# Performance work log

Measured on AMD Instinct MI355X. Metric: run time of the kernel, lower is better.

Reference implementation:

```python
import jax, jax.numpy as jnp
import numpy as np

N = 100000
E = 1600000
D = 128
H = 64
C = 10
G = 1024  # number of graphs in the batch


def setup_inputs() -> dict:
    key = jax.random.key(0)
    ks = jax.random.split(key, 12)
    x = jax.random.normal(ks[0], (N, D), dtype=jnp.float32)
    edge_index = jax.random.randint(ks[1], (2, E), 0, N, dtype=jnp.int64)
    batch = jnp.sort(jax.random.randint(ks[2], (N,), 0, G, dtype=jnp.int64))
    def glorot(k, fan_in, fan_out):
        s = jnp.sqrt(6.0 / (fan_in + fan_out))
        return jax.random.uniform(k, (fan_in, fan_out), jnp.float32, -s, s)
    W1 = glorot(ks[3], D, H); b1 = jnp.zeros((H,), jnp.float32)
    W2 = glorot(ks[4], H, H); b2 = jnp.zeros((H,), jnp.float32)
    W3 = glorot(ks[5], H, H); b3 = jnp.zeros((H,), jnp.float32)
    Wl = glorot(ks[6], H, C); bl = jnp.zeros((C,), jnp.float32)
    return {"x": x, "edge_index": edge_index, "batch": batch,
            "W1": W1, "b1": b1, "W2": W2, "b2": b2,
            "W3": W3, "b3": b3, "Wl": Wl, "bl": bl}


def gcn_conv(x, row, col, dinv, W, b):
    # PyG GCNConv: x' = D^-1/2 (A + I) D^-1/2 (x W) + b
    xw = x @ W                                   # (N, H)
    norm = dinv[row] * dinv[col]                 # (E+N,)
    msg = xw[row] * norm[:, None]                # gather + scale
    out = jax.ops.segment_sum(msg, col, num_segments=N)
    return out + b


def reference(x, edge_index, batch, W1, b1, W2, b2, W3, b3, Wl, bl):
    # add self loops once; normalization coefficients shared by all layers
    loop = jnp.arange(N, dtype=edge_index.dtype)
    row = jnp.concatenate([edge_index[0], loop])
    col = jnp.concatenate([edge_index[1], loop])
    deg = jax.ops.segment_sum(jnp.ones_like(col, dtype=x.dtype), col, num_segments=N)
    dinv = jnp.where(deg > 0, jax.lax.rsqrt(deg), 0.0)

    h = gcn_conv(x, row, col, dinv, W1, b1)
    h = gcn_conv(h, row, col, dinv, W2, b2)
    h = gcn_conv(h, row, col, dinv, W3, b3)

    # global mean pool over graphs
    sums = jax.ops.segment_sum(h, batch, num_segments=G)          # (G, H)
    cnts = jax.ops.segment_sum(jnp.ones((N,), h.dtype), batch, num_segments=G)
    pooled = sums / jnp.maximum(cnts, 1.0)[:, None]

    # dropout(p=0.5) is identity in eval mode
    return pooled @ Wl + bl                                        # (G, C)
```

## Files before the change

kernel.cpp:

```cpp
#include <hip/hip_runtime.h>

#define NN 100000
#define EE 1600000
#define DI 128
#define HH 64
#define CO 10
#define PADF 16
#define GG 1024
#define BSH 7
#define BNODES 128
#define NB ((NN + BNODES - 1) / BNODES)
#define TILE 4096
#define NT ((EE + TILE - 1) / TILE)
#define SN (NB * NT)
#define SCB 1024
#define NSB ((SN + SCB - 1) / SCB)
#define LPN 4
#define BT 256

__global__ __launch_bounds__(256) void k_front(const int* __restrict__ col,
                                               const float* __restrict__ W1, const float* __restrict__ W2,
                                               const float* __restrict__ W3, const float* __restrict__ Wl,
                                               const float* __restrict__ b1, const float* __restrict__ b2,
                                               const float* __restrict__ b3,
                                               const int* __restrict__ batch,
                                               int* __restrict__ cnt, float* __restrict__ Wf,
                                               float* __restrict__ cvec, int* __restrict__ gstart) {
    __shared__ float smem[1280];
    int bid = blockIdx.x, t = threadIdx.x;
    if (bid < NT) {
        int* h = (int*)smem;
        for (int i = t; i < NB; i += 256) h[i] = 0;
        __syncthreads();
        int base = bid * TILE, end = min(base + TILE, EE);
        for (int e = base + t; e < end; e += 256)
            atomicAdd(&h[__builtin_nontemporal_load(&col[e]) >> BSH], 1);
        __syncthreads();
        for (int i = t; i < NB; i += 256) cnt[i * NT + bid] = h[i];
    } else if (bid == NT) {
        float* M3l = smem;
        float* M23l = smem + 640;
        for (int i = t; i < HH * CO; i += 256) {
            int r = i / CO, c = i % CO; float s = 0.f;
            for (int k = 0; k < HH; ++k) s += W3[r * HH + k] * Wl[k * CO + c];
            M3l[i] = s;
        }
        __syncthreads();
        for (int i = t; i < HH * CO; i += 256) {
            int r = i / CO, c = i % CO; float s = 0.f;
            for (int k = 0; k < HH; ++k) s += W2[r * HH + k] * M3l[k * CO + c];
            M23l[i] = s;
        }
        __syncthreads();
        for (int i = t; i < DI * CO; i += 256) {
            int r = i / CO, c = i % CO; float s = 0.f;
            for (int k = 0; k < HH; ++k) s += W1[r * HH + k] * M23l[k * CO + c];
            Wf[i] = s;
        }
        if (t < CO) {
            float s1 = 0.f, s2 = 0.f, s3 = 0.f;
            for (int k = 0; k < HH; ++k) {
                s1 += b1[k] * M23l[k * CO + t];
                s2 += b2[k] * M3l[k * CO + t];
                s3 += b3[k] * Wl[k * CO + t];
            }
            cvec[t] = s1; cvec[CO + t] = s2; cvec[2 * CO + t] = s3;
        }
    } else {
        int g = (bid - NT - 1) * 256 + t;
        if (g <= GG) {
            int lo = 0, hi = NN;
            while (lo < hi) { int mid = (lo + hi) >> 1; if (batch[mid] < g) lo = mid + 1; else hi = mid; }
            gstart[g] = lo;
        }
    }
}

__global__ __launch_bounds__(SCB) void k_scanA(int* __restrict__ a, int* __restrict__ bsum) {
    __shared__ int s[SCB];
    int t = threadIdx.x, idx = blockIdx.x * SCB + t;
    int v = (idx < SN) ? a[idx] : 0;
    s[t] = v;
    __syncthreads();
    for (int off = 1; off < SCB; off <<= 1) {
        int u = (t >= off) ? s[t - off] : 0;
        __syncthreads();
        s[t] += u;
        __syncthreads();
    }
    if (idx < SN) a[idx] = s[t] - v;
    if (t == SCB - 1) bsum[blockIdx.x] = s[t];
}
__global__ __launch_bounds__(SCB) void k_scanC(int* __restrict__ a, const int* __restrict__ bsum) {
    __shared__ int red[SCB];
    int t = threadIdx.x, bid = blockIdx.x;
    int partial = 0;
    for (int i = t; i < bid; i += SCB) partial += bsum[i];
    red[t] = partial;
    __syncthreads();
    for (int off = SCB / 2; off > 0; off >>= 1) {
        if (t < off) red[t] += red[t + off];
        __syncthreads();
    }
    int idx = bid * SCB + t;
    if (idx < SN) a[idx] += red[0];
}

__global__ __launch_bounds__(256) void k_sxw(const int* __restrict__ row, const int* __restrict__ col,
                                             const int* __restrict__ S, unsigned* __restrict__ ebuf,
                                             const float* __restrict__ x, const float* __restrict__ Wf,
                                             float* __restrict__ as_) {
    __shared__ float smf[DI * CO];
    int* smi = (int*)smf;
    int bid = blockIdx.x, t = threadIdx.x;
    if (bid < NT) {
        for (int i = t; i < NB; i += 256) smi[i] = S[i * NT + bid];
        __syncthreads();
        int base = bid * TILE, end = min(base + TILE, EE);
        for (int e = base + t; e < end; e += 256) {
            int c = __builtin_nontemporal_load(&col[e]);
            int r = __builtin_nontemporal_load(&row[e]);
            int pos = atomicAdd(&smi[c >> BSH], 1);
            ebuf[pos] = ((unsigned)r << BSH) | (unsigned)(c & (BNODES - 1));
        }
    } else {
        for (int i = t; i < DI * CO; i += 256) smf[i] = Wf[i];
        __syncthreads();
        int gid = (bid - NT) * 256 + t;
        if (gid >= NN) return;
        int pr = gid >> 1, c0 = (gid & 1) * 5;
        int n0 = 2 * pr, n1 = n0 + 1;
        float a0[5] = {0, 0, 0, 0, 0}, a1[5] = {0, 0, 0, 0, 0};
        const float4* x0 = (const float4*)(x + (size_t)n0 * DI);
        const float4* x1 = (const float4*)(x + (size_t)n1 * DI);
#pragma unroll 4
        for (int d4 = 0; d4 < DI / 4; ++d4) {
            float4 u = x0[d4], v = x1[d4];
            const float* w = &smf[d4 * 4 * CO + c0];
#pragma unroll
            for (int c = 0; c < 5; ++c) {
                float w0 = w[c], w1 = w[CO + c], w2 = w[2 * CO + c], w3 = w[3 * CO + c];
                a0[c] += u.x * w0 + u.y * w1 + u.z * w2 + u.w * w3;
                a1[c] += v.x * w0 + v.y * w1 + v.z * w2 + v.w * w3;
            }
        }
        float* r0 = as_ + (size_t)n0 * PADF + c0;
        float* r1 = as_ + (size_t)n1 * PADF + c0;
#pragma unroll
        for (int c = 0; c < 5; ++c) { r0[c] = a0[c]; r1[c] = a1[c]; }
    }
}

__global__ __launch_bounds__(256) void k_bsort(const unsigned* __restrict__ ebuf, const int* __restrict__ S,
                                               int* __restrict__ srcIdx, int* __restrict__ rowptr_end,
                                               float* __restrict__ dinv) {
    __shared__ int cnt[BNODES];
    __shared__ int s[BNODES];
    __shared__ int ofs[BNODES];
    int t = threadIdx.x;
    int b = blockIdx.x;
    if (t < BNODES) cnt[t] = 0;
    __syncthreads();
    int beg = S[b * NT];
    int end = (b + 1 < NB) ? S[(b + 1) * NT] : EE;
    for (int e = beg + t; e < end; e += 256)
        atomicAdd(&cnt[__builtin_nontemporal_load(&ebuf[e]) & (BNODES - 1)], 1);
    __syncthreads();
    int v = 0;
    if (t < BNODES) { v = cnt[t]; s[t] = v; }
    __syncthreads();
    for (int off = 1; off < BNODES; off <<= 1) {
        int u = 0;
        if (t < BNODES && t >= off) u = s[t - off];
        __syncthreads();
        if (t < BNODES) s[t] += u;
        __syncthreads();
    }
    if (t < BNODES) {
        int n = (b << BSH) + t;
        if (n < NN) {
            dinv[n] = rsqrtf((float)(v + 1));
            rowptr_end[n] = beg + s[t];
        }
        ofs[t] = beg + s[t] - v;
    }
    __syncthreads();
    for (int e = beg + t; e < end; e += 256) {
        unsigned p = __builtin_nontemporal_load(&ebuf[e]);
        int pos = atomicAdd(&ofs[p & (BNODES - 1)], 1);
        srcIdx[pos] = (int)(p >> BSH);
    }
}

template <int MODE>
__global__ __launch_bounds__(256) void k_gather(const int* __restrict__ rowptr_end,
                                                const int* __restrict__ srcIdx,
                                                const float* __restrict__ src,
                                                const float* __restrict__ dinv,
                                                const float* __restrict__ cvec, int coff,
                                                float* __restrict__ dst) {
    int gid = blockIdx.x * 256 + threadIdx.x;
    int n = gid >> 2;
    int l = threadIdx.x & (LPN - 1);
    if (n >= NN) return;
    int beg = (n == 0) ? 0 : rowptr_end[n - 1];
    int end = rowptr_end[n];
    float acc[CO];
#pragma unroll
    for (int c = 0; c < CO; ++c) acc[c] = 0.f;
    for (int e = beg + l; e < end; e += LPN) {
        int s = __builtin_nontemporal_load(&srcIdx[e]);
        const float* sp = src + (size_t)s * PADF;
        float4 a = ((const float4*)sp)[0];
        float4 b = ((const float4*)sp)[1];
        float2 c2 = ((const float2*)(sp + 8))[0];
        if (MODE == 0) {
            float w = dinv[s];
            acc[0] += w * a.x; acc[1] += w * a.y; acc[2] += w * a.z; acc[3] += w * a.w;
            acc[4] += w * b.x; acc[5] += w * b.y; acc[6] += w * b.z; acc[7] += w * b.w;
            acc[8] += w * c2.x; acc[9] += w * c2.y;
        } else {
            acc[0] += a.x; acc[1] += a.y; acc[2] += a.z; acc[3] += a.w;
            acc[4] += b.x; acc[5] += b.y; acc[6] += b.z; acc[7] += b.w;
            acc[8] += c2.x; acc[9] += c2.y;
        }
    }
#pragma unroll
    for (int m = 1; m < LPN; m <<= 1) {
#pragma unroll
        for (int c = 0; c < CO; ++c) acc[c] += __shfl_xor(acc[c], m, 64);
    }
    if (l == 0) {
        float di = dinv[n];
        const float* selfp = src + (size_t)n * PADF;
        float4 sa = ((const float4*)selfp)[0];
        float4 sb = ((const float4*)selfp)[1];
        float2 sc = ((const float2*)(selfp + 8))[0];
        float self[CO] = {sa.x, sa.y, sa.z, sa.w, sb.x, sb.y, sb.z, sb.w, sc.x, sc.y};
        float o[CO];
#pragma unroll
        for (int c = 0; c < CO; ++c) {
            float sv = (MODE == 0) ? di * self[c] : self[c];
            float y = di * (acc[c] + sv) + cvec[coff + c];
            o[c] = (MODE == 2) ? y : y * di;
        }
        float* dp = dst + (size_t)n * PADF;
        ((float4*)dp)[0] = make_float4(o[0], o[1], o[2], o[3]);
        ((float4*)dp)[1] = make_float4(o[4], o[5], o[6], o[7]);
        ((float2*)(dp + 8))[0] = make_float2(o[8], o[9]);
    }
}

__global__ __launch_bounds__(64) void k_pool(const float* __restrict__ h,
                                             const int* __restrict__ gstart,
                                             const float* __restrict__ bl,
                                             float* __restrict__ out) {
    int g = blockIdx.x;
    int beg = gstart[g], end = gstart[g + 1];
    int l = threadIdx.x;
    float acc[CO];
#pragma unroll
    for (int c = 0; c < CO; ++c) acc[c] = 0.f;
    for (int n = beg + l; n < end; n += 64) {
        const float* sp = h + (size_t)n * PADF;
        float4 a = ((const float4*)sp)[0];
        float4 b = ((const float4*)sp)[1];
        float2 c2 = ((const float2*)(sp + 8))[0];
        acc[0] += a.x; acc[1] += a.y; acc[2] += a.z; acc[3] += a.w;
        acc[4] += b.x; acc[5] += b.y; acc[6] += b.z; acc[7] += b.w;
        acc[8] += c2.x; acc[9] += c2.y;
    }
#pragma unroll
    for (int m = 1; m < 64; m <<= 1) {
#pragma unroll
        for (int c = 0; c < CO; ++c) acc[c] += __shfl_xor(acc[c], m, 64);
    }
    if (l == 0) {
        float cf = fmaxf((float)(end - beg), 1.f);
#pragma unroll
        for (int c = 0; c < CO; ++c) out[(size_t)g * CO + c] = acc[c] / cf + bl[c];
    }
}

extern "C" void kernel_launch(void* const* d_in, const int* in_sizes, int n_in,
                              void* d_out, int out_size, void* d_ws, size_t ws_size,
                              hipStream_t stream) {
    const float* x    = (const float*)d_in[0];
    const int*   ei   = (const int*)d_in[1];
    const int*   batch= (const int*)d_in[2];
    const float* W1   = (const float*)d_in[3];
    const float* b1   = (const float*)d_in[4];
    const float* W2   = (const float*)d_in[5];
    const float* b2   = (const float*)d_in[6];
    const float* W3   = (const float*)d_in[7];
    const float* b3   = (const float*)d_in[8];
    const float* Wl   = (const float*)d_in[9];
    const float* bl   = (const float*)d_in[10];
    float* out = (float*)d_out;

    const int* row = ei;
    const int* col = ei + EE;

    float* ws = (float*)d_ws;
    size_t off = 0;
    auto alloc = [&](size_t elems) { size_t cur = off; off += (elems + 63) & ~(size_t)63; return cur; };
    float*    Wf      = ws + alloc(DI * CO);
    float*    cvec    = ws + alloc(3 * CO);
    float*    dinv    = ws + alloc(NN);
    int*      S       = (int*)(ws + alloc(SN));
    int*      bsum    = (int*)(ws + alloc(NSB + 64));
    unsigned* ebuf    = (unsigned*)(ws + alloc(EE));
    int*      srcIdx  = (int*)(ws + alloc(EE));
    int*      rowptr  = (int*)(ws + alloc(NN));
    float*    as_     = ws + alloc((size_t)NN * PADF);
    float*    bbuf    = ws + alloc((size_t)NN * PADF);
    int*      gstart  = (int*)(ws + alloc(GG + 1));
    (void)ws_size; (void)in_sizes; (void)n_in; (void)out_size;

    int gNL = ((NN * LPN) + BT - 1) / BT;
    int gFront = NT + 1 + (GG + 1 + BT - 1) / BT;
    int gSxw = NT + (NN + BT - 1) / BT;

    hipLaunchKernelGGL(k_front,    dim3(gFront), dim3(BT), 0, stream,
                       col, W1, W2, W3, Wl, b1, b2, b3, batch, S, Wf, cvec, gstart);
    hipLaunchKernelGGL(k_scanA,    dim3(NSB), dim3(SCB), 0, stream, S, bsum);
    hipLaunchKernelGGL(k_scanC,    dim3(NSB), dim3(SCB), 0, stream, S, bsum);
    hipLaunchKernelGGL(k_sxw,      dim3(gSxw), dim3(BT), 0, stream, row, col, S, ebuf, x, Wf, as_);
    hipLaunchKernelGGL(k_bsort,    dim3(NB),  dim3(BT), 0, stream, ebuf, S, srcIdx, rowptr, dinv);

    hipLaunchKernelGGL((k_gather<0>), dim3(gNL), dim3(BT), 0, stream, rowptr, srcIdx, as_,  dinv, cvec, 0,      bbuf);
    hipLaunchKernelGGL((k_gather<1>), dim3(gNL), dim3(BT), 0, stream, rowptr, srcIdx, bbuf, dinv, cvec, CO,     as_);
    hipLaunchKernelGGL((k_gather<2>), dim3(gNL), dim3(BT), 0, stream, rowptr, srcIdx, as_,  dinv, cvec, 2 * CO, bbuf);

    hipLaunchKernelGGL(k_pool, dim3(GG), dim3(64), 0, stream, bbuf, gstart, bl, out);
}
```

Baseline: 288.8 us.

## Split gather by feature quarter per lane instead of by edge

The gather kernel now gives each of the four lanes per node one float4 slice of the padded 16-float feature row, and every lane walks all edges of that node. Before, each lane took every fourth edge and read all ten channels, then the lanes combined results with a shuffle reduction. The new scheme removes the shuffle reduction and lets all lanes store in parallel, and the four lanes' loads of one row fall into one 64-byte segment. To keep the padding channels zero, the projection kernel now explicitly zeroes floats 10-15 of each row. In exchange, each lane loads every srcIdx and dinv entry redundantly and runs a serial loop over the node's full degree.

```diff
diff --git a/kernel.cpp b/kernel.cpp
--- a/kernel.cpp
+++ b/kernel.cpp
@@ -15,7 +15,6 @@
 #define SN (NB * NT)
 #define SCB 1024
 #define NSB ((SN + SCB - 1) / SCB)
-#define LPN 4
 #define BT 256
 
 __global__ __launch_bounds__(256) void k_front(const int* __restrict__ col,
@@ -148,6 +147,14 @@
         float* r1 = as_ + (size_t)n1 * PADF + c0;
 #pragma unroll
         for (int c = 0; c < 5; ++c) { r0[c] = a0[c]; r1[c] = a1[c]; }
+        if (c0) {
+            float* p0 = as_ + (size_t)n0 * PADF;
+            float* p1 = as_ + (size_t)n1 * PADF;
+            ((float2*)(p0 + 10))[0] = make_float2(0.f, 0.f);
+            ((float4*)(p0 + 12))[0] = make_float4(0.f, 0.f, 0.f, 0.f);
+            ((float2*)(p1 + 10))[0] = make_float2(0.f, 0.f);
+            ((float4*)(p1 + 12))[0] = make_float4(0.f, 0.f, 0.f, 0.f);
+        }
     }
 }
 
@@ -201,54 +208,40 @@
                                                 float* __restrict__ dst) {
     int gid = blockIdx.x * 256 + threadIdx.x;
     int n = gid >> 2;
-    int l = threadIdx.x & (LPN - 1);
+    int l = threadIdx.x & 3;
     if (n >= NN) return;
     int beg = (n == 0) ? 0 : rowptr_end[n - 1];
     int end = rowptr_end[n];
-    float acc[CO];
-#pragma unroll
-    for (int c = 0; c < CO; ++c) acc[c] = 0.f;
-    for (int e = beg + l; e < end; e += LPN) {
-        int s = __builtin_nontemporal_load(&srcIdx[e]);
-        const float* sp = src + (size_t)s * PADF;
-        float4 a = ((const float4*)sp)[0];
-        float4 b = ((const float4*)sp)[1];
-        float2 c2 = ((const float2*)(sp + 8))[0];
+    float4 acc = make_float4(0.f, 0.f, 0.f, 0.f);
+#pragma unroll 4
+    for (int e = beg; e < end; ++e) {
+        int s = srcIdx[e];
+        float4 v = ((const float4*)(src + (size_t)s * PADF))[l];
         if (MODE == 0) {
             float w = dinv[s];
-            acc[0] += w * a.x; acc[1] += w * a.y; acc[2] += w * a.z; acc[3] += w * a.w;
-            acc[4] += w * b.x; acc[5] += w * b.y; acc[6] += w * b.z; acc[7] += w * b.w;
-            acc[8] += w * c2.x; acc[9] += w * c2.y;
+            acc.x += w * v.x; acc.y += w * v.y; acc.z += w * v.z; acc.w += w * v.w;
         } else {
-            acc[0] += a.x; acc[1] += a.y; acc[2] += a.z; acc[3] += a.w;
-            acc[4] += b.x; acc[5] += b.y; acc[6] += b.z; acc[7] += b.w;
-            acc[8] += c2.x; acc[9] += c2.y;
-        }
-    }
-#pragma unroll
-    for (int m = 1; m < LPN; m <<= 1) {
-#pragma unroll
-        for (int c = 0; c < CO; ++c) acc[c] += __shfl_xor(acc[c], m, 64);
-    }
-    if (l == 0) {
-        float di = dinv[n];
-        const float* selfp = src + (size_t)n * PADF;
-        float4 sa = ((const float4*)selfp)[0];
-        float4 sb = ((const float4*)selfp)[1];
-        float2 sc = ((const float2*)(selfp + 8))[0];
-        float self[CO] = {sa.x, sa.y, sa.z, sa.w, sb.x, sb.y, sb.z, sb.w, sc.x, sc.y};
-        float o[CO];
-#pragma unroll
-        for (int c = 0; c < CO; ++c) {
-            float sv = (MODE == 0) ? di * self[c] : self[c];
-            float y = di * (acc[c] + sv) + cvec[coff + c];
-            o[c] = (MODE == 2) ? y : y * di;
-        }
-        float* dp = dst + (size_t)n * PADF;
-        ((float4*)dp)[0] = make_float4(o[0], o[1], o[2], o[3]);
-        ((float4*)dp)[1] = make_float4(o[4], o[5], o[6], o[7]);
-        ((float2*)(dp + 8))[0] = make_float2(o[8], o[9]);
-    }
+            acc.x += v.x; acc.y += v.y; acc.z += v.z; acc.w += v.w;
+        }
+    }
+    float di = dinv[n];
+    float4 sv = ((const float4*)(src + (size_t)n * PADF))[l];
+    if (MODE == 0) { sv.x *= di; sv.y *= di; sv.z *= di; sv.w *= di; }
+    float cv0, cv1, cv2, cv3;
+    {
+        int ch = 4 * l;
+        cv0 = (ch + 0 < CO) ? cvec[coff + ch + 0] : 0.f;
+        cv1 = (ch + 1 < CO) ? cvec[coff + ch + 1] : 0.f;
+        cv2 = (ch + 2 < CO) ? cvec[coff + ch + 2] : 0.f;
+        cv3 = (ch + 3 < CO) ? cvec[coff + ch + 3] : 0.f;
+    }
+    float4 o;
+    o.x = di * (acc.x + sv.x) + cv0;
+    o.y = di * (acc.y + sv.y) + cv1;
+    o.z = di * (acc.z + sv.z) + cv2;
+    o.w = di * (acc.w + sv.w) + cv3;
+    if (MODE != 2) { o.x *= di; o.y *= di; o.z *= di; o.w *= di; }
+    ((float4*)(dst + (size_t)n * PADF))[l] = o;
 }
 
 __global__ __launch_bounds__(64) void k_pool(const float* __restrict__ h,
@@ -317,7 +310,7 @@
     int*      gstart  = (int*)(ws + alloc(GG + 1));
     (void)ws_size; (void)in_sizes; (void)n_in; (void)out_size;
 
-    int gNL = ((NN * LPN) + BT - 1) / BT;
+    int gNL = ((NN * 4) + BT - 1) / BT;
     int gFront = NT + 1 + (GG + 1 + BT - 1) / BT;
     int gSxw = NT + (NN + BT - 1) / BT;
 
```

Measured after the change: 271.1 us. -6.1%, faster.
